# Performance work log

Hardware: AMD Instinct MI355X
Metric: run time of the kernel (lower is better)

Reference implementation:

```python
import jax, jax.numpy as jnp
import numpy as np

B, F, W, O, L_HID = 4096, 128, 128, 32, 2  # batch, input_dim, width, output_dim, layers-1


def setup_inputs() -> dict:
    key = jax.random.key(0)
    ks = jax.random.split(key, 7)
    s1 = 1.0  # fan_in=1 for first layer
    sw = 1.0 / np.sqrt(W)
    return {
        "x": jax.random.normal(ks[0], (B, F), dtype=jnp.float32),
        "W1": jax.random.normal(ks[1], (F, W), dtype=jnp.float32) * s1,
        "b1": jax.random.normal(ks[2], (F, W), dtype=jnp.float32) * 0.1,
        "Wh": jax.random.normal(ks[3], (L_HID, F, W, W), dtype=jnp.float32) * sw,
        "bh": jax.random.normal(ks[4], (L_HID, F, W), dtype=jnp.float32) * 0.1,
        "Wo": jax.random.normal(ks[5], (F, W, O), dtype=jnp.float32) * sw,
        "bo": jax.random.normal(ks[6], (F, O), dtype=jnp.float32) * 0.1,
    }


def reference(x, W1, b1, Wh, bh, Wo, bo):
    # Per-feature scalar-input MLPs, fused as grouped (block-diagonal) GEMMs.
    # First layer: Linear(1, width) per feature -> h[b,f,w] = x[b,f]*W1[f,w] + b1[f,w]
    h = jax.nn.relu(x[:, :, None] * W1[None, :, :] + b1[None, :, :])  # [B,F,W]
    # Hidden layers: Linear(width, width) per feature
    for l in range(Wh.shape[0]):
        h = jax.nn.relu(jnp.einsum("bfw,fwv->bfv", h, Wh[l]) + bh[l][None, :, :])
    # Output layer per feature, link_fn = identity, then sum over features (NGAM accumulate)
    per_feat = jnp.einsum("bfw,fwo->bfo", h, Wo) + bo[None, :, :]  # [B,F,O]
    return per_feat.sum(axis=1)  # [B,O]
```

## Files before the change

### kernel.cpp

```cpp
#include <hip/hip_runtime.h>

#define BATCH 4096
#define NF 128
#define NW 128
#define NO 32
#define MT 128
#define LDH 136

#define WH_ELEMS (2 * 128 * 128 * 128)
#define WO_ELEMS (128 * 128 * 32)

typedef _Float16 f16x8 __attribute__((ext_vector_type(8)));
typedef float f32x16 __attribute__((ext_vector_type(16)));

static __device__ __forceinline__ unsigned short f2h(float f) {
    return __builtin_bit_cast(unsigned short, (_Float16)f);
}
static __device__ __forceinline__ unsigned long long pack4rtz(float a, float b, float c, float d) {
    unsigned lo = __builtin_bit_cast(unsigned, __builtin_amdgcn_cvt_pkrtz(a, b));
    unsigned hi = __builtin_bit_cast(unsigned, __builtin_amdgcn_cvt_pkrtz(c, d));
    return (unsigned long long)lo | ((unsigned long long)hi << 32);
}

__global__ __launch_bounds__(256) void prep_weights4(
    const float* __restrict__ Wh, const float* __restrict__ Wo,
    const float* __restrict__ x, unsigned short* __restrict__ ws,
    float* __restrict__ out) {
    __shared__ __align__(16) unsigned char sm_raw[128 * 129 * 4];
    unsigned short* t_sm = (unsigned short*)sm_raw;
    float* ts = (float*)sm_raw;
    unsigned short* wh = ws;
    unsigned short* wo = ws + WH_ELEMS;
    float* xT = (float*)(ws + WH_ELEMS + WO_ELEMS);
    const int b = blockIdx.x;
    const int tid = threadIdx.x;
    if (b < 256) {
        const float* src = Wh + (size_t)b * 16384;
        for (int i = tid; i < 16384; i += 256) {
            int k = i >> 7, v = i & 127;
            t_sm[v * 138 + k] = f2h(src[i]);
        }
        __syncthreads();
        unsigned short* dst = wh + (size_t)b * 16384;
        for (int i = tid; i < 8192; i += 256) {
            int v = i >> 6, kp = i & 63;
            unsigned lo = t_sm[v * 138 + 2 * kp];
            unsigned hi = t_sm[v * 138 + 2 * kp + 1];
            *(unsigned*)&dst[v * 128 + 2 * kp] = lo | (hi << 16);
        }
    } else if (b < 384) {
        const int f = b - 256;
        const float* src = Wo + (size_t)f * 4096;
        for (int i = tid; i < 4096; i += 256) {
            int k = i >> 5, o = i & 31;
            t_sm[o * 138 + k] = f2h(src[i]);
        }
        __syncthreads();
        unsigned short* dst = wo + (size_t)f * 4096;
        for (int i = tid; i < 2048; i += 256) {
            int o = i >> 6, kp = i & 63;
            unsigned lo = t_sm[o * 138 + 2 * kp];
            unsigned hi = t_sm[o * 138 + 2 * kp + 1];
            *(unsigned*)&dst[o * 128 + 2 * kp] = lo | (hi << 16);
        }
    } else if (b < 400) {
        const int zb = b - 384;
        float4 z = (float4){0.f, 0.f, 0.f, 0.f};
        for (int i = zb * 256 + tid; i < BATCH * NO / 4; i += 16 * 256)
            *(float4*)&out[i * 4] = z;
    } else {
        const int mb = (b - 400) * 128;
        for (int i = tid; i < 128 * 128; i += 256) {
            int r = i >> 7, f = i & 127;
            ts[f * 129 + r] = x[(size_t)(mb + r) * NF + f];
        }
        __syncthreads();
        for (int i = tid; i < 128 * 128; i += 256) {
            int f = i >> 7, r = i & 127;
            xT[(size_t)f * BATCH + mb + r] = ts[f * 129 + r];
        }
    }
}

__global__ __launch_bounds__(256, 4) void ngam_fused(
    const float* __restrict__ W1, const float* __restrict__ b1,
    const float* __restrict__ bh, const float* __restrict__ bo,
    const unsigned short* __restrict__ ws, float* __restrict__ out) {
    __shared__ __align__(16) unsigned short h_sm[MT * LDH];
    const unsigned short* wh = ws;
    const unsigned short* wo = ws + WH_ELEMS;
    const float* xT = (const float*)(ws + WH_ELEMS + WO_ELEMS);

    const int bid   = blockIdx.x;
    const int lb    = (bid & 7) * 512 + (bid >> 3);
    const int f     = lb >> 5;
    const int m0    = (lb & 31) * MT;
    const int tid   = threadIdx.x;
    const int wave  = tid >> 6;
    const int lane  = tid & 63;
    const int l31   = lane & 31;
    const int khalf = lane >> 5;

    {
        int m = tid >> 1, c = tid & 1;
        float xv = xT[(size_t)f * BATCH + m0 + m];
        const float* w1r = &W1[f * NW];
        const float* b1r = &b1[f * NW];
        for (int jh = 0; jh < 2; ++jh) {
#pragma unroll
            for (int j = 0; j < 8; ++j) {
                int wq = c * 64 + (jh * 8 + j) * 4;
                float4 w1 = *(const float4*)&w1r[wq];
                float4 bb = *(const float4*)&b1r[wq];
                float v0 = fmaxf(xv * w1.x + bb.x, 0.0f);
                float v1 = fmaxf(xv * w1.y + bb.y, 0.0f);
                float v2 = fmaxf(xv * w1.z + bb.z, 0.0f);
                float v3 = fmaxf(xv * w1.w + bb.w, 0.0f);
                *(unsigned long long*)&h_sm[m * LDH + wq] = pack4rtz(v0, v1, v2, v3);
            }
        }
    }
    __syncthreads();

#pragma unroll
    for (int l = 0; l < 2; ++l) {
        const unsigned short* wp = wh + (size_t)(l * NF + f) * 16384;
        const float* bhl = bh + (size_t)(l * NF + f) * NW;

        f16x8 A[8];
#pragma unroll
        for (int ks = 0; ks < 8; ++ks)
            A[ks] = *(const f16x8*)&wp[(wave * 32 + l31) * 128 + ks * 16 + khalf * 8];

        f32x16 binit;
#pragma unroll
        for (int q = 0; q < 4; ++q) {
            float4 bb4 = *(const float4*)&bhl[wave * 32 + 8 * q + 4 * khalf];
            binit[4 * q + 0] = bb4.x; binit[4 * q + 1] = bb4.y;
            binit[4 * q + 2] = bb4.z; binit[4 * q + 3] = bb4.w;
        }
        f32x16 acc[4];
#pragma unroll
        for (int mt = 0; mt < 4; ++mt) acc[mt] = binit;

        __builtin_amdgcn_s_setprio(1);
#pragma unroll
        for (int mt = 0; mt < 4; ++mt) {
#pragma unroll
            for (int ks = 0; ks < 8; ++ks) {
                f16x8 bfr = *(const f16x8*)&h_sm[(mt * 32 + l31) * LDH + ks * 16 + khalf * 8];
                acc[mt] = __builtin_amdgcn_mfma_f32_32x32x16_f16(A[ks], bfr, acc[mt], 0, 0, 0);
            }
        }
        __builtin_amdgcn_s_setprio(0);
        __syncthreads();
#pragma unroll
        for (int mt = 0; mt < 4; ++mt)
#pragma unroll
            for (int q = 0; q < 4; ++q)
                *(unsigned long long*)&h_sm[(mt * 32 + l31) * LDH + wave * 32 + 8 * q + 4 * khalf] =
                    pack4rtz(fmaxf(acc[mt][4 * q + 0], 0.f), fmaxf(acc[mt][4 * q + 1], 0.f),
                             fmaxf(acc[mt][4 * q + 2], 0.f), fmaxf(acc[mt][4 * q + 3], 0.f));
        __syncthreads();
    }

    {
        const unsigned short* wop = wo + (size_t)f * 4096;
        const float* bof = bo + (size_t)f * NO;
        f16x8 Bo[8];
#pragma unroll
        for (int ks = 0; ks < 8; ++ks)
            Bo[ks] = *(const f16x8*)&wop[l31 * 128 + ks * 16 + khalf * 8];
        float bv = bof[l31];
        f32x16 acc2;
#pragma unroll
        for (int i = 0; i < 16; ++i) acc2[i] = bv;
        __builtin_amdgcn_s_setprio(1);
#pragma unroll
        for (int ks = 0; ks < 8; ++ks) {
            f16x8 a = *(const f16x8*)&h_sm[(wave * 32 + l31) * LDH + ks * 16 + khalf * 8];
            acc2 = __builtin_amdgcn_mfma_f32_32x32x16_f16(a, Bo[ks], acc2, 0, 0, 0);
        }
        __builtin_amdgcn_s_setprio(0);
#pragma unroll
        for (int r = 0; r < 16; ++r) {
            int row = m0 + wave * 32 + (r & 3) + 8 * (r >> 2) + 4 * khalf;
            atomicAdd(&out[(size_t)row * NO + l31], acc2[r]);
        }
    }
}

extern "C" void kernel_launch(void* const* d_in, const int* in_sizes, int n_in,
                              void* d_out, int out_size, void* d_ws, size_t ws_size,
                              hipStream_t stream) {
    const float* x  = (const float*)d_in[0];
    const float* W1 = (const float*)d_in[1];
    const float* b1 = (const float*)d_in[2];
    const float* Wh = (const float*)d_in[3];
    const float* bh = (const float*)d_in[4];
    const float* Wo = (const float*)d_in[5];
    const float* bo = (const float*)d_in[6];
    float* out = (float*)d_out;
    unsigned short* ws = (unsigned short*)d_ws;

    prep_weights4<<<432, 256, 0, stream>>>(Wh, Wo, x, ws, out);
    ngam_fused<<<NF * (BATCH / MT), 256, 0, stream>>>(W1, b1, bh, bo, ws, out);
}
```

Baseline: 99.74 us.

## Keep activations in registers across layers using permuted-K weight layout

Removes the shared-memory activation buffer and the barriers between layers. Each wave now keeps its own 32 batch rows in registers, and the MFMA output fragments are fed straight back as the B operand of the next layer. To make that work, the prep kernel permutes the K pairs of the fp16 weights so that the accumulator's row ordering matches the operand layout. The exchange is that every wave now streams the full 128x128 weight matrix from global/L2, where before each wave read a quarter slice and shared the activations through LDS, and register pressure goes up.

```diff
diff --git a/kernel.cpp b/kernel.cpp
--- a/kernel.cpp
+++ b/kernel.cpp
@@ -4,25 +4,27 @@
 #define NF 128
 #define NW 128
 #define NO 32
-#define MT 128
-#define LDH 136
 
 #define WH_ELEMS (2 * 128 * 128 * 128)
 #define WO_ELEMS (128 * 128 * 32)
 
 typedef _Float16 f16x8 __attribute__((ext_vector_type(8)));
 typedef float f32x16 __attribute__((ext_vector_type(16)));
+typedef unsigned u32x4 __attribute__((ext_vector_type(4)));
 
 static __device__ __forceinline__ unsigned short f2h(float f) {
     return __builtin_bit_cast(unsigned short, (_Float16)f);
 }
-static __device__ __forceinline__ unsigned long long pack4rtz(float a, float b, float c, float d) {
-    unsigned lo = __builtin_bit_cast(unsigned, __builtin_amdgcn_cvt_pkrtz(a, b));
-    unsigned hi = __builtin_bit_cast(unsigned, __builtin_amdgcn_cvt_pkrtz(c, d));
-    return (unsigned long long)lo | ((unsigned long long)hi << 32);
-}
-
-__global__ __launch_bounds__(256) void prep_weights4(
+static __device__ __forceinline__ unsigned pkrtz(float a, float b) {
+    return __builtin_bit_cast(unsigned, __builtin_amdgcn_cvt_pkrtz(a, b));
+}
+static __device__ __forceinline__ int ksrc_pair(int kp) {
+    int lp = kp & 7;
+    int sp = (lp & 1) | ((lp & 2) << 1) | ((lp & 4) >> 1);
+    return (kp & ~7) | sp;
+}
+
+__global__ __launch_bounds__(256) void prep_weights5(
     const float* __restrict__ Wh, const float* __restrict__ Wo,
     const float* __restrict__ x, unsigned short* __restrict__ ws,
     float* __restrict__ out) {
@@ -44,8 +46,9 @@
         unsigned short* dst = wh + (size_t)b * 16384;
         for (int i = tid; i < 8192; i += 256) {
             int v = i >> 6, kp = i & 63;
-            unsigned lo = t_sm[v * 138 + 2 * kp];
-            unsigned hi = t_sm[v * 138 + 2 * kp + 1];
+            int sk = ksrc_pair(kp);
+            unsigned lo = t_sm[v * 138 + 2 * sk];
+            unsigned hi = t_sm[v * 138 + 2 * sk + 1];
             *(unsigned*)&dst[v * 128 + 2 * kp] = lo | (hi << 16);
         }
     } else if (b < 384) {
@@ -59,8 +62,9 @@
         unsigned short* dst = wo + (size_t)f * 4096;
         for (int i = tid; i < 2048; i += 256) {
             int o = i >> 6, kp = i & 63;
-            unsigned lo = t_sm[o * 138 + 2 * kp];
-            unsigned hi = t_sm[o * 138 + 2 * kp + 1];
+            int sk = ksrc_pair(kp);
+            unsigned lo = t_sm[o * 138 + 2 * sk];
+            unsigned hi = t_sm[o * 138 + 2 * sk + 1];
             *(unsigned*)&dst[o * 128 + 2 * kp] = lo | (hi << 16);
         }
     } else if (b < 400) {
@@ -82,11 +86,49 @@
     }
 }
 
+static __device__ __forceinline__ void hidden_layer(
+    unsigned (&hin)[8][4], unsigned (&hout)[8][4],
+    const unsigned short* __restrict__ wp, const float* __restrict__ bhl,
+    int l31, int khalf) {
+#pragma unroll
+    for (int vt = 0; vt < 4; ++vt) {
+        f32x16 acc;
+#pragma unroll
+        for (int q = 0; q < 4; ++q) {
+            float4 bb4 = *(const float4*)&bhl[32 * vt + 8 * q + 4 * khalf];
+            acc[4 * q + 0] = bb4.x; acc[4 * q + 1] = bb4.y;
+            acc[4 * q + 2] = bb4.z; acc[4 * q + 3] = bb4.w;
+        }
+        __builtin_amdgcn_s_setprio(1);
+#pragma unroll
+        for (int kh = 0; kh < 2; ++kh) {
+            f16x8 A[4];
+#pragma unroll
+            for (int k2 = 0; k2 < 4; ++k2)
+                A[k2] = *(const f16x8*)&wp[(32 * vt + l31) * 128 + (kh * 4 + k2) * 16 + khalf * 8];
+#pragma unroll
+            for (int k2 = 0; k2 < 4; ++k2) {
+                int ks = kh * 4 + k2;
+                u32x4 bu = (u32x4){hin[ks][0], hin[ks][1], hin[ks][2], hin[ks][3]};
+                acc = __builtin_amdgcn_mfma_f32_32x32x16_f16(
+                    A[k2], __builtin_bit_cast(f16x8, bu), acc, 0, 0, 0);
+            }
+        }
+        __builtin_amdgcn_s_setprio(0);
+#pragma unroll
+        for (int qp = 0; qp < 2; ++qp) {
+            hout[2 * vt + qp][0] = pkrtz(fmaxf(acc[8 * qp + 0], 0.f), fmaxf(acc[8 * qp + 1], 0.f));
+            hout[2 * vt + qp][1] = pkrtz(fmaxf(acc[8 * qp + 2], 0.f), fmaxf(acc[8 * qp + 3], 0.f));
+            hout[2 * vt + qp][2] = pkrtz(fmaxf(acc[8 * qp + 4], 0.f), fmaxf(acc[8 * qp + 5], 0.f));
+            hout[2 * vt + qp][3] = pkrtz(fmaxf(acc[8 * qp + 6], 0.f), fmaxf(acc[8 * qp + 7], 0.f));
+        }
+    }
+}
+
 __global__ __launch_bounds__(256, 4) void ngam_fused(
     const float* __restrict__ W1, const float* __restrict__ b1,
     const float* __restrict__ bh, const float* __restrict__ bo,
     const unsigned short* __restrict__ ws, float* __restrict__ out) {
-    __shared__ __align__(16) unsigned short h_sm[MT * LDH];
     const unsigned short* wh = ws;
     const unsigned short* wo = ws + WH_ELEMS;
     const float* xT = (const float*)(ws + WH_ELEMS + WO_ELEMS);
@@ -94,97 +136,58 @@
     const int bid   = blockIdx.x;
     const int lb    = (bid & 7) * 512 + (bid >> 3);
     const int f     = lb >> 5;
-    const int m0    = (lb & 31) * MT;
-    const int tid   = threadIdx.x;
-    const int wave  = tid >> 6;
-    const int lane  = tid & 63;
+    const int m0w   = (lb & 31) * 128 + (threadIdx.x >> 6) * 32;
+    const int lane  = threadIdx.x & 63;
     const int l31   = lane & 31;
     const int khalf = lane >> 5;
 
+    unsigned hA[8][4], hB[8][4];
+
     {
-        int m = tid >> 1, c = tid & 1;
-        float xv = xT[(size_t)f * BATCH + m0 + m];
+        float xv = xT[(size_t)f * BATCH + m0w + l31];
         const float* w1r = &W1[f * NW];
         const float* b1r = &b1[f * NW];
-        for (int jh = 0; jh < 2; ++jh) {
-#pragma unroll
-            for (int j = 0; j < 8; ++j) {
-                int wq = c * 64 + (jh * 8 + j) * 4;
-                float4 w1 = *(const float4*)&w1r[wq];
-                float4 bb = *(const float4*)&b1r[wq];
-                float v0 = fmaxf(xv * w1.x + bb.x, 0.0f);
-                float v1 = fmaxf(xv * w1.y + bb.y, 0.0f);
-                float v2 = fmaxf(xv * w1.z + bb.z, 0.0f);
-                float v3 = fmaxf(xv * w1.w + bb.w, 0.0f);
-                *(unsigned long long*)&h_sm[m * LDH + wq] = pack4rtz(v0, v1, v2, v3);
-            }
-        }
-    }
-    __syncthreads();
-
-#pragma unroll
-    for (int l = 0; l < 2; ++l) {
-        const unsigned short* wp = wh + (size_t)(l * NF + f) * 16384;
-        const float* bhl = bh + (size_t)(l * NF + f) * NW;
-
-        f16x8 A[8];
-#pragma unroll
-        for (int ks = 0; ks < 8; ++ks)
-            A[ks] = *(const f16x8*)&wp[(wave * 32 + l31) * 128 + ks * 16 + khalf * 8];
-
-        f32x16 binit;
-#pragma unroll
-        for (int q = 0; q < 4; ++q) {
-            float4 bb4 = *(const float4*)&bhl[wave * 32 + 8 * q + 4 * khalf];
-            binit[4 * q + 0] = bb4.x; binit[4 * q + 1] = bb4.y;
-            binit[4 * q + 2] = bb4.z; binit[4 * q + 3] = bb4.w;
-        }
-        f32x16 acc[4];
-#pragma unroll
-        for (int mt = 0; mt < 4; ++mt) acc[mt] = binit;
-
-        __builtin_amdgcn_s_setprio(1);
-#pragma unroll
-        for (int mt = 0; mt < 4; ++mt) {
-#pragma unroll
-            for (int ks = 0; ks < 8; ++ks) {
-                f16x8 bfr = *(const f16x8*)&h_sm[(mt * 32 + l31) * LDH + ks * 16 + khalf * 8];
-                acc[mt] = __builtin_amdgcn_mfma_f32_32x32x16_f16(A[ks], bfr, acc[mt], 0, 0, 0);
-            }
-        }
-        __builtin_amdgcn_s_setprio(0);
-        __syncthreads();
-#pragma unroll
-        for (int mt = 0; mt < 4; ++mt)
-#pragma unroll
-            for (int q = 0; q < 4; ++q)
-                *(unsigned long long*)&h_sm[(mt * 32 + l31) * LDH + wave * 32 + 8 * q + 4 * khalf] =
-                    pack4rtz(fmaxf(acc[mt][4 * q + 0], 0.f), fmaxf(acc[mt][4 * q + 1], 0.f),
-                             fmaxf(acc[mt][4 * q + 2], 0.f), fmaxf(acc[mt][4 * q + 3], 0.f));
-        __syncthreads();
-    }
+#pragma unroll
+        for (int ks = 0; ks < 8; ++ks) {
+            float4 wa = *(const float4*)&w1r[ks * 16 + 4 * khalf];
+            float4 ba = *(const float4*)&b1r[ks * 16 + 4 * khalf];
+            float4 wb = *(const float4*)&w1r[ks * 16 + 8 + 4 * khalf];
+            float4 bb = *(const float4*)&b1r[ks * 16 + 8 + 4 * khalf];
+            hA[ks][0] = pkrtz(fmaxf(xv * wa.x + ba.x, 0.f), fmaxf(xv * wa.y + ba.y, 0.f));
+            hA[ks][1] = pkrtz(fmaxf(xv * wa.z + ba.z, 0.f), fmaxf(xv * wa.w + ba.w, 0.f));
+            hA[ks][2] = pkrtz(fmaxf(xv * wb.x + bb.x, 0.f), fmaxf(xv * wb.y + bb.y, 0.f));
+            hA[ks][3] = pkrtz(fmaxf(xv * wb.z + bb.z, 0.f), fmaxf(xv * wb.w + bb.w, 0.f));
+        }
+    }
+
+    hidden_layer(hA, hB, wh + (size_t)(0 * NF + f) * 16384, bh + (size_t)(0 * NF + f) * NW, l31, khalf);
+    hidden_layer(hB, hA, wh + (size_t)(1 * NF + f) * 16384, bh + (size_t)(1 * NF + f) * NW, l31, khalf);
 
     {
         const unsigned short* wop = wo + (size_t)f * 4096;
-        const float* bof = bo + (size_t)f * NO;
-        f16x8 Bo[8];
-#pragma unroll
-        for (int ks = 0; ks < 8; ++ks)
-            Bo[ks] = *(const f16x8*)&wop[l31 * 128 + ks * 16 + khalf * 8];
-        float bv = bof[l31];
+        float bv = bo[f * NO + l31];
         f32x16 acc2;
 #pragma unroll
         for (int i = 0; i < 16; ++i) acc2[i] = bv;
         __builtin_amdgcn_s_setprio(1);
 #pragma unroll
-        for (int ks = 0; ks < 8; ++ks) {
-            f16x8 a = *(const f16x8*)&h_sm[(wave * 32 + l31) * LDH + ks * 16 + khalf * 8];
-            acc2 = __builtin_amdgcn_mfma_f32_32x32x16_f16(a, Bo[ks], acc2, 0, 0, 0);
+        for (int kh = 0; kh < 2; ++kh) {
+            f16x8 Bo[4];
+#pragma unroll
+            for (int k2 = 0; k2 < 4; ++k2)
+                Bo[k2] = *(const f16x8*)&wop[l31 * 128 + (kh * 4 + k2) * 16 + khalf * 8];
+#pragma unroll
+            for (int k2 = 0; k2 < 4; ++k2) {
+                int ks = kh * 4 + k2;
+                u32x4 au = (u32x4){hA[ks][0], hA[ks][1], hA[ks][2], hA[ks][3]};
+                acc2 = __builtin_amdgcn_mfma_f32_32x32x16_f16(
+                    __builtin_bit_cast(f16x8, au), Bo[k2], acc2, 0, 0, 0);
+            }
         }
         __builtin_amdgcn_s_setprio(0);
 #pragma unroll
         for (int r = 0; r < 16; ++r) {
-            int row = m0 + wave * 32 + (r & 3) + 8 * (r >> 2) + 4 * khalf;
+            int row = m0w + (r & 3) + 8 * (r >> 2) + 4 * khalf;
             atomicAdd(&out[(size_t)row * NO + l31], acc2[r]);
         }
     }
@@ -203,6 +206,6 @@
     float* out = (float*)d_out;
     unsigned short* ws = (unsigned short*)d_ws;
 
-    prep_weights4<<<432, 256, 0, stream>>>(Wh, Wo, x, ws, out);
-    ngam_fused<<<NF * (BATCH / MT), 256, 0, stream>>>(W1, b1, bh, bo, ws, out);
-}
+    prep_weights5<<<432, 256, 0, stream>>>(Wh, Wo, x, ws, out);
+    ngam_fused<<<4096, 256, 0, stream>>>(W1, b1, bh, bo, ws, out);
+}
```

After: 183.4 us. 83.9% more time.
